# Kernel tuning notes

Measured on AMD Instinct MI355X. Metric: run time of the kernel, lower is better.

## Reference

```python
import jax, jax.numpy as jnp
import numpy as np

D_MODEL = 1024

def setup_inputs() -> dict:
    key = jax.random.key(0)
    ks = jax.random.split(key, 7)
    B, S, D = 4, 2048, D_MODEL
    scale = 1.0 / np.sqrt(D)
    x = jax.random.normal(ks[0], (B, S, D), dtype=jnp.float32)
    Wq = jax.random.normal(ks[1], (D, D), dtype=jnp.float32) * scale
    bq = jnp.zeros((D,), dtype=jnp.float32)
    Wk = jax.random.normal(ks[2], (D, D), dtype=jnp.float32) * scale
    bk = jnp.zeros((D,), dtype=jnp.float32)
    Wv = jax.random.normal(ks[3], (D, D), dtype=jnp.float32) * scale
    bv = jnp.zeros((D,), dtype=jnp.float32)
    return {"x": x, "Wq": Wq, "bq": bq, "Wk": Wk, "bk": bk, "Wv": Wv, "bv": bv}

def reference(x, Wq, bq, Wk, bk, Wv, bv):
    # Single-head attention; scale = 1/sqrt(d_model) as in the torch module (self.d_k = d_model).
    d_k = x.shape[-1]
    q = jnp.einsum('bsd,de->bse', x, Wq) + bq
    k = jnp.einsum('bsd,de->bse', x, Wk) + bk
    v = jnp.einsum('bsd,de->bse', x, Wv) + bv
    scores = jnp.einsum('bqd,bkd->bqk', q, k) / jnp.sqrt(jnp.asarray(d_k, x.dtype))
    attn = jax.nn.softmax(scores, axis=-1)
    return jnp.einsum('bqk,bkd->bqd', attn, v)
```

## Files before the change

### kernel.cpp

```cpp
#include <hip/hip_runtime.h>
#include <hip/hip_bf16.h>

#define DM 1024
#define SEQ 2048
#define NBATCH 4

using f32x4 = __attribute__((ext_vector_type(4))) float;
using s16x8 = __attribute__((ext_vector_type(8))) short;
using u16x4 = __attribute__((ext_vector_type(4))) unsigned short;
using u16x8 = __attribute__((ext_vector_type(8))) unsigned short;

__device__ __forceinline__ unsigned short f2bf(float f) {
  union { float f; unsigned u; } v; v.f = f;
  return (unsigned short)((v.u + 0x7fffu + ((v.u >> 16) & 1u)) >> 16);
}


__global__ void cvt_x(const float* __restrict__ X, unsigned short* __restrict__ XB) {
  const int i = blockIdx.x * 256 + threadIdx.x;
  const f32x4* p = (const f32x4*)X;
  f32x4 a = p[2 * i], b = p[2 * i + 1];
  u16x8 o;
#pragma unroll
  for (int q = 0; q < 4; q++) { o[q] = f2bf(a[q]); o[4 + q] = f2bf(b[q]); }
  *(u16x8*)(XB + (size_t)i * 8) = o;
}

__global__ void transpose_w(const float* __restrict__ Wq, const float* __restrict__ Wk,
                            const float* __restrict__ Wv, unsigned short* __restrict__ WT) {
  const int seg = blockIdx.z;
  const float* W = (seg == 0) ? Wq : (seg == 1) ? Wk : Wv;
  unsigned short* out = WT + (size_t)seg * DM * DM;
  __shared__ float t[32][33];
  const int k0 = blockIdx.y * 32, n0 = blockIdx.x * 32;
  const int tr = threadIdx.x >> 5, tc = threadIdx.x & 31;
#pragma unroll
  for (int p = 0; p < 4; p++) {
    int r = tr + p * 8;
    t[r][tc] = W[(size_t)(k0 + r) * DM + n0 + tc];
  }
  __syncthreads();
#pragma unroll
  for (int p = 0; p < 4; p++) {
    int r = tr + p * 8;
    out[(size_t)(n0 + r) * DM + k0 + tc] = f2bf(t[tc][r]);
  }
}

template <int MODE, int LDA, int LDB, int KDIM>
__global__ void gemm_nt(const unsigned short* __restrict__ A,
                        const unsigned short* __restrict__ B,
                        void* __restrict__ C0,
                        unsigned short* __restrict__ C1,
                        unsigned short* __restrict__ C2,
                        const float* __restrict__ bq,
                        const float* __restrict__ bk,
                        const float* __restrict__ bv) {
  __shared__ unsigned short lA[128 * 64];
  __shared__ unsigned short lB[128 * 64];

  const int tid = threadIdx.x;
  const int w = tid >> 6;
  const int L = tid & 63;
  const int wm = w & 1, wn = w >> 1;
  const int bz = blockIdx.z;
  const int tileM = blockIdx.y * 128, tileN = blockIdx.x * 128;

  const unsigned short* Ab = A;
  const unsigned short* Bb = B;
  if (MODE == 1) { Ab += (size_t)bz * SEQ * DM; Bb += (size_t)bz * SEQ * DM; }
  if (MODE == 2) { Ab += (size_t)bz * SEQ * SEQ; Bb += (size_t)bz * DM * SEQ; }

  const int srow = tid >> 3;
  const int pch = tid & 7;
  const int gch = pch ^ (srow & 7);
  const unsigned short* gA = Ab + (size_t)(tileM + srow) * LDA + gch * 8;
  const unsigned short* gB = Bb + (size_t)(tileN + srow) * LDB + gch * 8;
  unsigned short* wA = &lA[srow * 64 + pch * 8];
  unsigned short* wB = &lB[srow * 64 + pch * 8];

  u16x8 rA[4], rB[4];
#define LOADT(kt) do {                                                         \
    const size_t kk_ = (size_t)(kt) * 64;                                      \
    _Pragma("unroll")                                                          \
    for (int i_ = 0; i_ < 4; i_++) {                                           \
      rA[i_] = *(const u16x8*)(gA + (size_t)i_ * 32 * LDA + kk_);              \
      rB[i_] = *(const u16x8*)(gB + (size_t)i_ * 32 * LDB + kk_);              \
    }                                                                          \
  } while (0)
#define WRITET() do {                                                          \
    _Pragma("unroll")                                                          \
    for (int i_ = 0; i_ < 4; i_++) {                                           \
      *(u16x8*)(wA + i_ * 32 * 64) = rA[i_];                                   \
      *(u16x8*)(wB + i_ * 32 * 64) = rB[i_];                                   \
    }                                                                          \
  } while (0)

  f32x4 acc[4][4];
#pragma unroll
  for (int i = 0; i < 4; i++)
#pragma unroll
    for (int j = 0; j < 4; j++) acc[i][j] = (f32x4){0.f, 0.f, 0.f, 0.f};

  const int rl = L & 15;
  const int qh = L >> 4;
  const int sw = L & 7;

  constexpr int NK = KDIM / 64;
  LOADT(0);
  WRITET();
  __syncthreads();

  for (int k = 0; k < NK; ++k) {
    if (k + 1 < NK) LOADT(k + 1);

#pragma unroll
    for (int s = 0; s < 2; s++) {
      const int pc = ((s * 4 + qh) ^ sw) * 8;
      s16x8 av[4], bv4[4];
#pragma unroll
      for (int i = 0; i < 4; i++)
        av[i] = *(const s16x8*)&lA[(wm * 64 + i * 16 + rl) * 64 + pc];
#pragma unroll
      for (int j = 0; j < 4; j++)
        bv4[j] = *(const s16x8*)&lB[(wn * 64 + j * 16 + rl) * 64 + pc];
#pragma unroll
      for (int i = 0; i < 4; i++)
#pragma unroll
        for (int j = 0; j < 4; j++)
          acc[i][j] = __builtin_amdgcn_mfma_f32_16x16x32_bf16(av[i], bv4[j], acc[i][j], 0, 0, 0);
    }

    if (k + 1 < NK) {
      __builtin_amdgcn_s_waitcnt(0xC07F);
      __builtin_amdgcn_sched_barrier(0);
      __builtin_amdgcn_s_barrier();
      __builtin_amdgcn_sched_barrier(0);
      WRITET();
      __syncthreads();
    }
  }
#undef LOADT
#undef WRITET

#pragma unroll
  for (int i = 0; i < 4; i++) {
    const int gm0 = tileM + wm * 64 + i * 16 + (L >> 4) * 4;
#pragma unroll
    for (int j = 0; j < 4; j++) {
      const int gn = tileN + wn * 64 + j * 16 + (L & 15);
      if (MODE == 0) {
        const int seg = gn >> 10;
        const int colin = gn & 1023;
        if (seg == 0) {
          const float bias = bq[colin];
          unsigned short* Q = (unsigned short*)C0;
#pragma unroll
          for (int r = 0; r < 4; r++) Q[(size_t)(gm0 + r) * DM + colin] = f2bf(acc[i][j][r] + bias);
        } else if (seg == 1) {
          const float bias = bk[colin];
#pragma unroll
          for (int r = 0; r < 4; r++) C1[(size_t)(gm0 + r) * DM + colin] = f2bf(acc[i][j][r] + bias);
        } else {
          const float bias = bv[colin];
          u16x4 pk;
#pragma unroll
          for (int r = 0; r < 4; r++) pk[r] = f2bf(acc[i][j][r] + bias);
          const int b = gm0 >> 11, s0 = gm0 & 2047;
          *(u16x4*)(C2 + ((size_t)((b << 10) + colin)) * SEQ + s0) = pk;
        }
      } else if (MODE == 1) {
        float* S = (float*)C0 + (size_t)bz * SEQ * SEQ;
#pragma unroll
        for (int r = 0; r < 4; r++) S[(size_t)(gm0 + r) * SEQ + gn] = acc[i][j][r] * 0.03125f;
      } else {
        float* O = (float*)C0 + (size_t)bz * SEQ * DM;
#pragma unroll
        for (int r = 0; r < 4; r++) O[(size_t)(gm0 + r) * DM + gn] = acc[i][j][r];
      }
    }
  }
}

__global__ void softmax_k(const float* __restrict__ S, unsigned short* __restrict__ P) {
  const int row = blockIdx.x;
  const float* src = S + (size_t)row * SEQ;
  const int t = threadIdx.x;
  f32x4 a = *(const f32x4*)(src + t * 8);
  f32x4 b = *(const f32x4*)(src + t * 8 + 4);
  float m = fmaxf(fmaxf(fmaxf(a[0], a[1]), fmaxf(a[2], a[3])),
                  fmaxf(fmaxf(b[0], b[1]), fmaxf(b[2], b[3])));
#pragma unroll
  for (int o = 32; o > 0; o >>= 1) m = fmaxf(m, __shfl_down(m, o, 64));
  __shared__ float redm[4], reds[4];
  if ((t & 63) == 0) redm[t >> 6] = m;
  __syncthreads();
  m = fmaxf(fmaxf(redm[0], redm[1]), fmaxf(redm[2], redm[3]));
  float e[8]; float s = 0.f;
#pragma unroll
  for (int q = 0; q < 4; q++) { e[q] = __expf(a[q] - m); s += e[q]; }
#pragma unroll
  for (int q = 0; q < 4; q++) { e[4 + q] = __expf(b[q] - m); s += e[4 + q]; }
#pragma unroll
  for (int o = 32; o > 0; o >>= 1) s += __shfl_down(s, o, 64);
  if ((t & 63) == 0) reds[t >> 6] = s;
  __syncthreads();
  s = reds[0] + reds[1] + reds[2] + reds[3];
  const float inv = 1.0f / s;
  u16x8 o8;
#pragma unroll
  for (int q = 0; q < 8; q++) o8[q] = f2bf(e[q] * inv);
  *(u16x8*)(P + (size_t)row * SEQ + t * 8) = o8;
}

extern "C" void kernel_launch(void* const* d_in, const int* in_sizes, int n_in,
                              void* d_out, int out_size, void* d_ws, size_t ws_size,
                              hipStream_t stream) {
  (void)in_sizes; (void)n_in; (void)out_size; (void)ws_size;
  const float* x  = (const float*)d_in[0];
  const float* Wq = (const float*)d_in[1];
  const float* bq = (const float*)d_in[2];
  const float* Wk = (const float*)d_in[3];
  const float* bk = (const float*)d_in[4];
  const float* Wv = (const float*)d_in[5];
  const float* bv = (const float*)d_in[6];
  float* out = (float*)d_out;
  char* ws = (char*)d_ws;
  unsigned short* xb = (unsigned short*)(ws + 0);
  unsigned short* wt = (unsigned short*)(ws + 16777216);
  unsigned short* qb = (unsigned short*)(ws + 23068672);
  unsigned short* kb = (unsigned short*)(ws + 39845888);
  unsigned short* vt = (unsigned short*)(ws + 56623104);
  float*          S  = (float*)         (ws + 73400320);
  unsigned short* P  = (unsigned short*)(ws + 140509184);

  cvt_x<<<4096, 256, 0, stream>>>(x, xb);
  transpose_w<<<dim3(32, 32, 3), 256, 0, stream>>>(Wq, Wk, Wv, wt);
  gemm_nt<0, 1024, 1024, 1024><<<dim3(24, 64, 1), 256, 0, stream>>>(
      xb, wt, (void*)qb, kb, vt, bq, bk, bv);
  gemm_nt<1, 1024, 1024, 1024><<<dim3(16, 16, 4), 256, 0, stream>>>(
      qb, kb, (void*)S, nullptr, nullptr, nullptr, nullptr, nullptr);
  softmax_k<<<8192, 256, 0, stream>>>(S, P);
  gemm_nt<2, 2048, 2048, 2048><<<dim3(8, 16, 4), 256, 0, stream>>>(
      P, vt, (void*)out, nullptr, nullptr, nullptr, nullptr, nullptr);
}
```

Baseline: 267.8 us.

## Fuse softmax into QK^T epilogue with per-tile stats and rescale in PV GEMM

The QK^T GEMM now computes a local row max and exp-sum for each 128-column tile, writes unnormalized bf16 probabilities directly, and stores the per-tile statistics. A small combine kernel turns these into cross-tile rescale factors, and the PV GEMM rescales its accumulators every two k-steps (every 128 columns) and applies the final normalization in the epilogue. This removes the fp32 score matrix round-trip and the separate softmax kernel, in exchange for extra reductions and barriers in the QK epilogue, a tiny extra launch, and per-tile rescaling FLOPs in the PV loop.

New measurement: 344.6 us. 28.7% more time.

```diff
diff --git a/kernel.cpp b/kernel.cpp
--- a/kernel.cpp
+++ b/kernel.cpp
@@ -47,6 +47,27 @@
   }
 }
 
+__global__ void combine_k(const float* __restrict__ ms, const float* __restrict__ ss,
+                          float* __restrict__ T) {
+  const int idx = blockIdx.x * 256 + threadIdx.x;
+  const float* m = ms + (size_t)idx * 16;
+  const float* s = ss + (size_t)idx * 16;
+  float mv[16];
+#pragma unroll
+  for (int t = 0; t < 16; t++) mv[t] = m[t];
+  float M = mv[0];
+#pragma unroll
+  for (int t = 1; t < 16; t++) M = fmaxf(M, mv[t]);
+  float L = 0.f;
+#pragma unroll
+  for (int t = 0; t < 16; t++) L += s[t] * __expf(mv[t] - M);
+  float* o = T + (size_t)idx * 17;
+  o[0] = 1.0f;
+#pragma unroll
+  for (int t = 1; t < 16; t++) o[t] = __expf(mv[t - 1] - mv[t]);
+  o[16] = __expf(mv[15] - M) / L;
+}
+
 template <int MODE, int LDA, int LDB, int KDIM>
 __global__ void gemm_nt(const unsigned short* __restrict__ A,
                         const unsigned short* __restrict__ B,
@@ -55,7 +76,10 @@
                         unsigned short* __restrict__ C2,
                         const float* __restrict__ bq,
                         const float* __restrict__ bk,
-                        const float* __restrict__ bv) {
+                        const float* __restrict__ bv,
+                        float* __restrict__ sm,
+                        float* __restrict__ sv,
+                        const float* __restrict__ Tt) {
   __shared__ unsigned short lA[128 * 64];
   __shared__ unsigned short lB[128 * 64];
 
@@ -63,6 +87,7 @@
   const int w = tid >> 6;
   const int L = tid & 63;
   const int wm = w & 1, wn = w >> 1;
+  const int qd = L >> 4, ll = L & 15;
   const int bz = blockIdx.z;
   const int tileM = blockIdx.y * 128, tileN = blockIdx.x * 128;
 
@@ -102,9 +127,17 @@
 #pragma unroll
     for (int j = 0; j < 4; j++) acc[i][j] = (f32x4){0.f, 0.f, 0.f, 0.f};
 
-  const int rl = L & 15;
-  const int qh = L >> 4;
   const int sw = L & 7;
+
+  float tTn[4][4];
+  const float* Tp = nullptr;
+  if (MODE == 2) {
+    Tp = Tt + ((size_t)bz * SEQ + tileM + wm * 64) * 17;
+#pragma unroll
+    for (int i = 0; i < 4; i++)
+#pragma unroll
+      for (int r = 0; r < 4; r++) tTn[i][r] = Tp[(i * 16 + qd * 4 + r) * 17 + 1];
+  }
 
   constexpr int NK = KDIM / 64;
   LOADT(0);
@@ -112,18 +145,32 @@
   __syncthreads();
 
   for (int k = 0; k < NK; ++k) {
+    if (MODE == 2 && k >= 2 && (k & 1) == 0) {
+#pragma unroll
+      for (int i = 0; i < 4; i++)
+#pragma unroll
+        for (int j = 0; j < 4; j++)
+#pragma unroll
+          for (int r = 0; r < 4; r++) acc[i][j][r] *= tTn[i][r];
+      const int tn = (k >> 1) + 1;
+#pragma unroll
+      for (int i = 0; i < 4; i++)
+#pragma unroll
+        for (int r = 0; r < 4; r++) tTn[i][r] = Tp[(i * 16 + qd * 4 + r) * 17 + tn];
+    }
+
     if (k + 1 < NK) LOADT(k + 1);
 
 #pragma unroll
     for (int s = 0; s < 2; s++) {
-      const int pc = ((s * 4 + qh) ^ sw) * 8;
+      const int pc = ((s * 4 + qd) ^ sw) * 8;
       s16x8 av[4], bv4[4];
 #pragma unroll
       for (int i = 0; i < 4; i++)
-        av[i] = *(const s16x8*)&lA[(wm * 64 + i * 16 + rl) * 64 + pc];
+        av[i] = *(const s16x8*)&lA[(wm * 64 + i * 16 + ll) * 64 + pc];
 #pragma unroll
       for (int j = 0; j < 4; j++)
-        bv4[j] = *(const s16x8*)&lB[(wn * 64 + j * 16 + rl) * 64 + pc];
+        bv4[j] = *(const s16x8*)&lB[(wn * 64 + j * 16 + ll) * 64 + pc];
 #pragma unroll
       for (int i = 0; i < 4; i++)
 #pragma unroll
@@ -143,13 +190,13 @@
 #undef LOADT
 #undef WRITET
 
-#pragma unroll
-  for (int i = 0; i < 4; i++) {
-    const int gm0 = tileM + wm * 64 + i * 16 + (L >> 4) * 4;
-#pragma unroll
-    for (int j = 0; j < 4; j++) {
-      const int gn = tileN + wn * 64 + j * 16 + (L & 15);
-      if (MODE == 0) {
+  if (MODE == 0) {
+#pragma unroll
+    for (int i = 0; i < 4; i++) {
+      const int gm0 = tileM + wm * 64 + i * 16 + qd * 4;
+#pragma unroll
+      for (int j = 0; j < 4; j++) {
+        const int gn = tileN + wn * 64 + j * 16 + ll;
         const int seg = gn >> 10;
         const int colin = gn & 1023;
         if (seg == 0) {
@@ -169,48 +216,105 @@
           const int b = gm0 >> 11, s0 = gm0 & 2047;
           *(u16x4*)(C2 + ((size_t)((b << 10) + colin)) * SEQ + s0) = pk;
         }
-      } else if (MODE == 1) {
-        float* S = (float*)C0 + (size_t)bz * SEQ * SEQ;
-#pragma unroll
-        for (int r = 0; r < 4; r++) S[(size_t)(gm0 + r) * SEQ + gn] = acc[i][j][r] * 0.03125f;
-      } else {
-        float* O = (float*)C0 + (size_t)bz * SEQ * DM;
-#pragma unroll
-        for (int r = 0; r < 4; r++) O[(size_t)(gm0 + r) * DM + gn] = acc[i][j][r];
-      }
-    }
-  }
-}
-
-__global__ void softmax_k(const float* __restrict__ S, unsigned short* __restrict__ P) {
-  const int row = blockIdx.x;
-  const float* src = S + (size_t)row * SEQ;
-  const int t = threadIdx.x;
-  f32x4 a = *(const f32x4*)(src + t * 8);
-  f32x4 b = *(const f32x4*)(src + t * 8 + 4);
-  float m = fmaxf(fmaxf(fmaxf(a[0], a[1]), fmaxf(a[2], a[3])),
-                  fmaxf(fmaxf(b[0], b[1]), fmaxf(b[2], b[3])));
-#pragma unroll
-  for (int o = 32; o > 0; o >>= 1) m = fmaxf(m, __shfl_down(m, o, 64));
-  __shared__ float redm[4], reds[4];
-  if ((t & 63) == 0) redm[t >> 6] = m;
-  __syncthreads();
-  m = fmaxf(fmaxf(redm[0], redm[1]), fmaxf(redm[2], redm[3]));
-  float e[8]; float s = 0.f;
-#pragma unroll
-  for (int q = 0; q < 4; q++) { e[q] = __expf(a[q] - m); s += e[q]; }
-#pragma unroll
-  for (int q = 0; q < 4; q++) { e[4 + q] = __expf(b[q] - m); s += e[4 + q]; }
-#pragma unroll
-  for (int o = 32; o > 0; o >>= 1) s += __shfl_down(s, o, 64);
-  if ((t & 63) == 0) reds[t >> 6] = s;
-  __syncthreads();
-  s = reds[0] + reds[1] + reds[2] + reds[3];
-  const float inv = 1.0f / s;
-  u16x8 o8;
-#pragma unroll
-  for (int q = 0; q < 8; q++) o8[q] = f2bf(e[q] * inv);
-  *(u16x8*)(P + (size_t)row * SEQ + t * 8) = o8;
+      }
+    }
+  } else if (MODE == 1) {
+#pragma unroll
+    for (int i = 0; i < 4; i++)
+#pragma unroll
+      for (int j = 0; j < 4; j++)
+#pragma unroll
+        for (int r = 0; r < 4; r++) acc[i][j][r] *= 0.03125f;
+
+    __syncthreads();
+    float* pmx = (float*)lA;
+    float* psm = (float*)lA + 256;
+
+    float wmax[4][4];
+#pragma unroll
+    for (int i = 0; i < 4; i++)
+#pragma unroll
+      for (int r = 0; r < 4; r++) {
+        float v = fmaxf(fmaxf(acc[i][0][r], acc[i][1][r]), fmaxf(acc[i][2][r], acc[i][3][r]));
+#pragma unroll
+        for (int m = 1; m < 16; m <<= 1) v = fmaxf(v, __shfl_xor(v, m, 16));
+        wmax[i][r] = v;
+      }
+    if (ll == 0) {
+#pragma unroll
+      for (int i = 0; i < 4; i++)
+#pragma unroll
+        for (int r = 0; r < 4; r++)
+          pmx[wn * 128 + wm * 64 + i * 16 + qd * 4 + r] = wmax[i][r];
+    }
+    __syncthreads();
+    float mt[4][4];
+#pragma unroll
+    for (int i = 0; i < 4; i++)
+#pragma unroll
+      for (int r = 0; r < 4; r++) {
+        const int row = wm * 64 + i * 16 + qd * 4 + r;
+        mt[i][r] = fmaxf(pmx[row], pmx[128 + row]);
+      }
+    float wsum[4][4];
+#pragma unroll
+    for (int i = 0; i < 4; i++)
+#pragma unroll
+      for (int r = 0; r < 4; r++) {
+        float s = 0.f;
+#pragma unroll
+        for (int j = 0; j < 4; j++) {
+          float e = __expf(acc[i][j][r] - mt[i][r]);
+          acc[i][j][r] = e;
+          s += e;
+        }
+#pragma unroll
+        for (int m = 1; m < 16; m <<= 1) s += __shfl_xor(s, m, 16);
+        wsum[i][r] = s;
+      }
+    if (ll == 0) {
+#pragma unroll
+      for (int i = 0; i < 4; i++)
+#pragma unroll
+        for (int r = 0; r < 4; r++)
+          psm[wn * 128 + wm * 64 + i * 16 + qd * 4 + r] = wsum[i][r];
+    }
+    __syncthreads();
+    if (wn == 0 && ll == 0) {
+#pragma unroll
+      for (int i = 0; i < 4; i++)
+#pragma unroll
+        for (int r = 0; r < 4; r++) {
+          const int row = wm * 64 + i * 16 + qd * 4 + r;
+          const size_t sidx = ((size_t)bz * SEQ + tileM + row) * 16 + blockIdx.x;
+          sm[sidx] = mt[i][r];
+          sv[sidx] = psm[row] + psm[128 + row];
+        }
+    }
+    unsigned short* P = (unsigned short*)C0 + (size_t)bz * SEQ * SEQ;
+#pragma unroll
+    for (int i = 0; i < 4; i++)
+#pragma unroll
+      for (int r = 0; r < 4; r++) {
+        const int row_g = tileM + wm * 64 + i * 16 + qd * 4 + r;
+        unsigned short* dst = P + (size_t)row_g * SEQ + tileN + wn * 64 + ll;
+#pragma unroll
+        for (int j = 0; j < 4; j++) dst[j * 16] = f2bf(acc[i][j][r]);
+      }
+  } else {
+    float* O = (float*)C0 + (size_t)bz * SEQ * DM;
+#pragma unroll
+    for (int i = 0; i < 4; i++) {
+      const int gm0 = tileM + wm * 64 + i * 16 + qd * 4;
+#pragma unroll
+      for (int j = 0; j < 4; j++) {
+        const int gn = tileN + wn * 64 + j * 16 + ll;
+#pragma unroll
+        for (int r = 0; r < 4; r++)
+          O[(size_t)(gm0 + r) * DM + gn] = acc[i][j][r] * tTn[i][r];
+      }
+    }
+  }
 }
 
 extern "C" void kernel_launch(void* const* d_in, const int* in_sizes, int n_in,
@@ -231,16 +335,18 @@
   unsigned short* qb = (unsigned short*)(ws + 23068672);
   unsigned short* kb = (unsigned short*)(ws + 39845888);
   unsigned short* vt = (unsigned short*)(ws + 56623104);
-  float*          S  = (float*)         (ws + 73400320);
-  unsigned short* P  = (unsigned short*)(ws + 140509184);
+  unsigned short* P  = (unsigned short*)(ws + 73400320);
+  float*          ms = (float*)(ws + 106954752);
+  float*          ss = (float*)(ws + 107479040);
+  float*          Tt = (float*)(ws + 108003328);
 
   cvt_x<<<4096, 256, 0, stream>>>(x, xb);
   transpose_w<<<dim3(32, 32, 3), 256, 0, stream>>>(Wq, Wk, Wv, wt);
   gemm_nt<0, 1024, 1024, 1024><<<dim3(24, 64, 1), 256, 0, stream>>>(
-      xb, wt, (void*)qb, kb, vt, bq, bk, bv);
+      xb, wt, (void*)qb, kb, vt, bq, bk, bv, nullptr, nullptr, nullptr);
   gemm_nt<1, 1024, 1024, 1024><<<dim3(16, 16, 4), 256, 0, stream>>>(
-      qb, kb, (void*)S, nullptr, nullptr, nullptr, nullptr, nullptr);
-  softmax_k<<<8192, 256, 0, stream>>>(S, P);
+      qb, kb, (void*)P, nullptr, nullptr, nullptr, nullptr, nullptr, ms, ss, nullptr);
+  combine_k<<<32, 256, 0, stream>>>(ms, ss, Tt);
   gemm_nt<2, 2048, 2048, 2048><<<dim3(8, 16, 4), 256, 0, stream>>>(
-      P, vt, (void*)out, nullptr, nullptr, nullptr, nullptr, nullptr);
-}
+      P, vt, (void*)out, nullptr, nullptr, nullptr, nullptr, nullptr, nullptr, nullptr, Tt);
+}
```
